# Kernel tuning notes

Hardware: AMD Instinct MI355X
Metric: run time of the kernel (lower is better)

## Reference

```python
import jax, jax.numpy as jnp
import numpy as np

NUM_HEADS = 16
ROPE_BASE = 50.0


def _apply_rope(x):
    # x: [b, s, h, d]; torchtune-style rotary embedding with base=ROPE_BASE
    b, s, h, d = x.shape
    inv_freq = 1.0 / (ROPE_BASE ** (jnp.arange(0, d, 2, dtype=jnp.float32) / d))  # [d/2]
    angles = jnp.arange(s, dtype=jnp.float32)[:, None] * inv_freq[None, :]         # [s, d/2]
    cos = jnp.cos(angles)[None, :, None, :]  # [1, s, 1, d/2]
    sin = jnp.sin(angles)[None, :, None, :]
    xr = x.reshape(b, s, h, d // 2, 2)
    x0, x1 = xr[..., 0], xr[..., 1]
    out = jnp.stack([x0 * cos - x1 * sin, x1 * cos + x0 * sin], axis=-1)
    return out.reshape(b, s, h, d).astype(x.dtype)


def setup_inputs() -> dict:
    key = jax.random.key(0)
    k1, k2, k3 = jax.random.split(key, 3)
    B, S, D = 2, 2048, 1024
    x = jax.random.normal(k1, (B, S, D), dtype=jnp.float32)
    w_qkv = jax.random.normal(k2, (3 * D, D), dtype=jnp.float32) * (D ** -0.5)
    w_out = jax.random.normal(k3, (D, D), dtype=jnp.float32) * (D ** -0.5)
    b_out = jnp.zeros((D,), dtype=jnp.float32)
    return {"x": x, "w_qkv": w_qkv, "w_out": w_out, "b_out": b_out}


def reference(x, w_qkv, w_out, b_out):
    B, S, D = x.shape
    H = NUM_HEADS
    dk = D // H

    qkv = x @ w_qkv.T                       # [b, s, 3D]
    q, k, v = jnp.split(qkv, 3, axis=-1)
    q = q.reshape(B, S, H, dk)
    k = k.reshape(B, S, H, dk)
    q = _apply_rope(q)
    k = _apply_rope(k)
    q = q.transpose(0, 2, 1, 3)             # [b, h, s, d]
    k = k.transpose(0, 2, 1, 3)
    v = v.reshape(B, S, H, dk).transpose(0, 2, 1, 3)

    scale = 1.0 / jnp.sqrt(jnp.asarray(dk, dtype=x.dtype))
    scores = jnp.einsum('bhsd,bhtd->bhst', q, k) * scale  # [b, h, s, s]
    # additive diagonal mask: -inf on the diagonal (blocks self-attention)
    eye = jnp.eye(S, dtype=bool)
    scores = jnp.where(eye[None, None], -jnp.inf, scores)
    attn = jax.nn.softmax(scores, axis=-1)
    out = jnp.einsum('bhst,bhtd->bhsd', attn, v)          # [b, h, s, d]
    out = out.transpose(0, 2, 1, 3).reshape(B, S, D)
    return out @ w_out.T + b_out
```

## Files before the change

kernel.cpp:

```cpp
#include <hip/hip_runtime.h>
#include <hip/hip_bf16.h>
#include <math.h>
#include <type_traits>

#define D_MODEL 1024
#define NHEADS  16
#define DK      64
#define SEQ     2048
#define BATCH   2
#define QTILE   128

typedef __attribute__((ext_vector_type(8)))  short  short8;
typedef __attribute__((ext_vector_type(8)))  unsigned short ushort8;
typedef __attribute__((ext_vector_type(4)))  float  floatx4;
typedef __attribute__((ext_vector_type(16))) float  floatx16;

__device__ __forceinline__ unsigned short f2bf(float f) {
    union { float f; unsigned int u; } v; v.f = f;
    unsigned int u = v.u;
    return (unsigned short)((u + 0x7FFFu + ((u >> 16) & 1u)) >> 16);
}
__device__ __forceinline__ float bf2f(unsigned short u) {
    union { unsigned int u; float f; } v; v.u = ((unsigned int)u) << 16;
    return v.f;
}
__device__ __forceinline__ unsigned int fau(float f) {
    union { float f; unsigned int u; } v; v.f = f; return v.u;
}

__device__ __forceinline__ void gload_lds16(const unsigned short* g, unsigned short* l) {
    __builtin_amdgcn_global_load_lds((__attribute__((address_space(1))) const void*)g,
                                     (__attribute__((address_space(3))) void*)l,
                                     16, 0, 0);
}

#define X8 ((BATCH * SEQ * D_MODEL) / 8)
#define W8 ((3 * D_MODEL * D_MODEL) / 8)
#define O8 ((D_MODEL * D_MODEL) / 8)
__global__ __launch_bounds__(256) void pack_all(const float* __restrict__ x,
                                                const float* __restrict__ wq,
                                                const float* __restrict__ wo,
                                                unsigned short* __restrict__ xb,
                                                unsigned short* __restrict__ wqb,
                                                unsigned short* __restrict__ wob) {
    const int t = blockIdx.x * blockDim.x + threadIdx.x;
    const float* src; unsigned short* dst; int idx;
    if (t < X8)           { src = x;  dst = xb;  idx = t; }
    else if (t < X8 + W8) { src = wq; dst = wqb; idx = t - X8; }
    else if (t < X8 + W8 + O8) { src = wo; dst = wob; idx = t - X8 - W8; }
    else return;
    const float4 a = ((const float4*)src)[2 * idx];
    const float4 b = ((const float4*)src)[2 * idx + 1];
    short8 o;
    o[0] = (short)f2bf(a.x); o[1] = (short)f2bf(a.y);
    o[2] = (short)f2bf(a.z); o[3] = (short)f2bf(a.w);
    o[4] = (short)f2bf(b.x); o[5] = (short)f2bf(b.y);
    o[6] = (short)f2bf(b.z); o[7] = (short)f2bf(b.w);
    ((short8*)dst)[idx] = o;
}

#define QKV_M 4096
#define QKV_N 3072
#define QKV_K 1024
#define QKV_NT (QKV_K / 64)

__global__ __launch_bounds__(512, 2) void gemm_qkv_8ph(const unsigned short* __restrict__ A,
                                                        const unsigned short* __restrict__ B,
                                                        unsigned short* __restrict__ C) {
    __shared__ __align__(16) unsigned short As[2][256][64];
    __shared__ __align__(16) unsigned short Bs[2][256][64];

    const int tid  = threadIdx.x;
    const int w    = tid >> 6;
    const int lane = tid & 63;
    const int quad = lane >> 4;
    const int lcol = lane & 15;
    const int wr   = w >> 2;
    const int wc   = w & 3;

    const int f  = blockIdx.x;
    const int wg = (f & 7) * 24 + (f >> 3);
    const int tn = (wg % (QKV_N / 256)) * 256;
    const int tm = (wg / (QKV_N / 256)) * 256;

    const int srow8 = lane >> 3;
    const int sj    = lane & 7;

    auto stageA = [&](int buf, int kt, int mh) {
#pragma unroll
        for (int c = 0; c < 2; ++c) {
            const int r0 = mh * 64 + c * 128 + w * 8;
            const int r  = r0 + srow8;
            gload_lds16(A + (size_t)(tm + r) * QKV_K + kt * 64 + ((sj ^ (r & 7)) * 8),
                        &As[buf][r0][0]);
        }
    };
    auto stageB = [&](int buf, int kt, int nh) {
#pragma unroll
        for (int c = 0; c < 2; ++c) {
            const int rho0 = c * 64 + w * 8;
            const int r0   = (rho0 >> 5) * 64 + nh * 32 + (rho0 & 31);
            const int r    = r0 + srow8;
            gload_lds16(B + (size_t)(tn + r) * QKV_K + kt * 64 + ((sj ^ (r & 7)) * 8),
                        &Bs[buf][r0][0]);
        }
    };

    floatx4 acc[8][4];
#pragma unroll
    for (int i = 0; i < 8; ++i)
#pragma unroll
        for (int j = 0; j < 4; ++j) acc[i][j] = (floatx4){0.f, 0.f, 0.f, 0.f};

    auto do_phase = [&](int buf, auto mhc, auto nhc, auto stager) {
        constexpr int mh = decltype(mhc)::value;
        constexpr int nh = decltype(nhc)::value;
        asm volatile("s_waitcnt vmcnt(4)" ::: "memory");
        __builtin_amdgcn_s_barrier();
        asm volatile("" ::: "memory");
        short8 a[4][2], bfr[2][2];
#pragma unroll
        for (int i = 0; i < 4; ++i)
#pragma unroll
            for (int kk = 0; kk < 2; ++kk) {
                const int r = wr * 128 + mh * 64 + i * 16 + lcol;
                a[i][kk] = *(const short8*)&As[buf][r][((kk * 4 + quad) ^ (r & 7)) * 8];
            }
#pragma unroll
        for (int j = 0; j < 2; ++j)
#pragma unroll
            for (int kk = 0; kk < 2; ++kk) {
                const int r = wc * 64 + nh * 32 + j * 16 + lcol;
                bfr[j][kk] = *(const short8*)&Bs[buf][r][((kk * 4 + quad) ^ (r & 7)) * 8];
            }
        stager();
        __builtin_amdgcn_s_setprio(1);
#pragma unroll
        for (int i = 0; i < 4; ++i)
#pragma unroll
            for (int j = 0; j < 2; ++j)
#pragma unroll
                for (int kk = 0; kk < 2; ++kk)
                    acc[mh * 4 + i][nh * 2 + j] = __builtin_amdgcn_mfma_f32_16x16x32_bf16(
                        a[i][kk], bfr[j][kk], acc[mh * 4 + i][nh * 2 + j], 0, 0, 0);
        __builtin_amdgcn_s_setprio(0);
    };

    using IC0 = std::integral_constant<int, 0>;
    using IC1 = std::integral_constant<int, 1>;

    stageA(0, 0, 0); stageB(0, 0, 0); stageB(0, 0, 1); stageA(0, 0, 1);

    for (int t = 0; t < QKV_NT; ++t) {
        const int buf = t & 1, nb = buf ^ 1;
        const int kn = (t + 1 == QKV_NT) ? 0 : t + 1;
        do_phase(buf, IC0{}, IC0{}, [&] { stageA(nb, kn, 0); });
        do_phase(buf, IC0{}, IC1{}, [&] { stageB(nb, kn, 0); });
        do_phase(buf, IC1{}, IC0{}, [&] { stageB(nb, kn, 1); });
        do_phase(buf, IC1{}, IC1{}, [&] { stageA(nb, kn, 1); });
    }

#pragma unroll
    for (int i = 0; i < 8; ++i) {
#pragma unroll
        for (int rr = 0; rr < 4; ++rr) {
            const int row = tm + wr * 128 + i * 16 + quad * 4 + rr;
#pragma unroll
            for (int jf = 0; jf < 4; ++jf) {
                const int col = tn + wc * 64 + jf * 16 + lcol;
                C[(size_t)row * QKV_N + col] = f2bf(acc[i][jf][rr]);
            }
        }
    }
}

#define OUT_M 4096
#define OUT_N 1024
#define OUT_K 1024
#define OUT_NT (OUT_K / 64)

__global__ __launch_bounds__(512, 2) void gemm_out_8ph(const unsigned short* __restrict__ A,
                                                       const unsigned short* __restrict__ B,
                                                       const float* __restrict__ bias,
                                                       float* __restrict__ C) {
    __shared__ __align__(16) unsigned short As[2][128][64];
    __shared__ __align__(16) unsigned short Bs[2][128][64];

    const int tid  = threadIdx.x;
    const int w    = tid >> 6;
    const int lane = tid & 63;
    const int quad = lane >> 4;
    const int lcol = lane & 15;
    const int wr   = w >> 2;
    const int wc   = w & 3;

    const int f  = blockIdx.x;
    const int wg = (f & 7) * 32 + (f >> 3);
    const int tn = (wg & 7) * 128;
    const int tm = (wg >> 3) * 128;

    const int srow8 = lane >> 3;
    const int sj    = lane & 7;

    auto stageA = [&](int buf, int kt, int mh) {
        const int r0 = (w & 3) * 8 + mh * 32 + (w >> 2) * 64;
        const int r  = r0 + srow8;
        gload_lds16(A + (size_t)(tm + r) * OUT_K + kt * 64 + ((sj ^ (r & 7)) * 8),
                    &As[buf][r0][0]);
    };
    auto stageB = [&](int buf, int kt, int nh) {
        const int r0 = (w >> 1) * 32 + nh * 16 + (w & 1) * 8;
        const int r  = r0 + srow8;
        gload_lds16(B + (size_t)(tn + r) * OUT_K + kt * 64 + ((sj ^ (r & 7)) * 8),
                    &Bs[buf][r0][0]);
    };

    floatx4 acc[4][2];
#pragma unroll
    for (int i = 0; i < 4; ++i)
#pragma unroll
        for (int j = 0; j < 2; ++j) acc[i][j] = (floatx4){0.f, 0.f, 0.f, 0.f};

    auto do_phase = [&](int buf, auto mhc, auto nhc, auto stager) {
        constexpr int mh = decltype(mhc)::value;
        constexpr int nh = decltype(nhc)::value;
        asm volatile("s_waitcnt vmcnt(2)" ::: "memory");
        __builtin_amdgcn_s_barrier();
        asm volatile("" ::: "memory");
        short8 a[2][2], bfr[2];
#pragma unroll
        for (int i = 0; i < 2; ++i)
#pragma unroll
            for (int kk = 0; kk < 2; ++kk) {
                const int r = wr * 64 + mh * 32 + i * 16 + lcol;
                a[i][kk] = *(const short8*)&As[buf][r][((kk * 4 + quad) ^ (r & 7)) * 8];
            }
#pragma unroll
        for (int kk = 0; kk < 2; ++kk) {
            const int r = wc * 32 + nh * 16 + lcol;
            bfr[kk] = *(const short8*)&Bs[buf][r][((kk * 4 + quad) ^ (r & 7)) * 8];
        }
        stager();
        __builtin_amdgcn_s_setprio(1);
#pragma unroll
        for (int i = 0; i < 2; ++i)
#pragma unroll
            for (int kk = 0; kk < 2; ++kk)
                acc[mh * 2 + i][nh] = __builtin_amdgcn_mfma_f32_16x16x32_bf16(
                    a[i][kk], bfr[kk], acc[mh * 2 + i][nh], 0, 0, 0);
        __builtin_amdgcn_s_setprio(0);
    };

    using IC0 = std::integral_constant<int, 0>;
    using IC1 = std::integral_constant<int, 1>;

    stageA(0, 0, 0); stageB(0, 0, 0); stageB(0, 0, 1); stageA(0, 0, 1);

    for (int t = 0; t < OUT_NT; ++t) {
        const int buf = t & 1, nb = buf ^ 1;
        const int kn = (t + 1 == OUT_NT) ? 0 : t + 1;
        do_phase(buf, IC0{}, IC0{}, [&] { stageA(nb, kn, 0); });
        do_phase(buf, IC0{}, IC1{}, [&] { stageB(nb, kn, 0); });
        do_phase(buf, IC1{}, IC0{}, [&] { stageB(nb, kn, 1); });
        do_phase(buf, IC1{}, IC1{}, [&] { stageA(nb, kn, 1); });
    }

#pragma unroll
    for (int i = 0; i < 4; ++i) {
#pragma unroll
        for (int rr = 0; rr < 4; ++rr) {
            const int row = tm + wr * 64 + i * 16 + quad * 4 + rr;
#pragma unroll
            for (int j = 0; j < 2; ++j) {
                const int col = tn + wc * 32 + j * 16 + lcol;
                C[(size_t)row * OUT_N + col] = acc[i][j][rr] + bias[col];
            }
        }
    }
}

__global__ __launch_bounds__(256) void rope_vtrans(const unsigned short* __restrict__ qkvb,
                                                   unsigned short* __restrict__ Qb,
                                                   unsigned short* __restrict__ Kb,
                                                   unsigned short* __restrict__ Vtg) {
    const int st = blockIdx.x, h = blockIdx.y, b = blockIdx.z;
    const int tid = threadIdx.x;
    const int s0 = st * 64;

    const int i  = tid & 31;
    const int r0 = tid >> 5;
    const float inv_freq = exp2f(-(2.0f * (float)i / (float)DK) * log2f(50.0f));
    const float QSCALE = 0.125f * 1.44269504f;
#pragma unroll
    for (int pass = 0; pass < 8; ++pass) {
        const int s = s0 + r0 + pass * 8;
        const size_t in_base = ((size_t)(b * SEQ + s)) * (3 * D_MODEL) + h * DK + 2 * i;
        const float q0 = bf2f(qkvb[in_base]),           q1 = bf2f(qkvb[in_base + 1]);
        const float k0 = bf2f(qkvb[in_base + D_MODEL]), k1 = bf2f(qkvb[in_base + D_MODEL + 1]);
        float sn, cs;
        __sincosf((float)s * inv_freq, &sn, &cs);
        const size_t ob = (((size_t)(b * NHEADS + h)) * SEQ + s) * DK + 2 * i;
        const unsigned int qw = (unsigned int)f2bf((q0 * cs - q1 * sn) * QSCALE)
                              | ((unsigned int)f2bf((q1 * cs + q0 * sn) * QSCALE) << 16);
        const unsigned int kw = (unsigned int)f2bf(k0 * cs - k1 * sn)
                              | ((unsigned int)f2bf(k1 * cs + k0 * sn) << 16);
        *(unsigned int*)&Qb[ob] = qw;
        *(unsigned int*)&Kb[ob] = kw;
    }

    __shared__ unsigned short Lt[64][65];
    const int r = tid >> 3;
    const int c = (tid & 7) * 8;
    const size_t in_row = ((size_t)(b * SEQ + s0 + r)) * (3 * D_MODEL) + 2 * D_MODEL + h * DK + c;
    const ushort8 v0 = *(const ushort8*)&qkvb[in_row];
    const ushort8 v1 = *(const ushort8*)&qkvb[in_row + (size_t)32 * (3 * D_MODEL)];
    const int u0 = r, u1 = r + 32;
    const int kc0 = (u0 & 48) | (8 * ((u0 >> 2) & 1) + (u0 & 3) + 4 * ((u0 >> 3) & 1));
    const int kc1 = (u1 & 48) | (8 * ((u1 >> 2) & 1) + (u1 & 3) + 4 * ((u1 >> 3) & 1));
#pragma unroll
    for (int j = 0; j < 8; ++j) Lt[c + j][kc0] = v0[j];
#pragma unroll
    for (int j = 0; j < 8; ++j) Lt[c + j][kc1] = v1[j];
    __syncthreads();
    const size_t bh = (size_t)(b * NHEADS + h);
    ushort8 o0, o1;
#pragma unroll
    for (int j = 0; j < 8; ++j) { o0[j] = Lt[r][c + j]; o1[j] = Lt[r + 32][c + j]; }
    unsigned short* orow = Vtg + (bh * DK + r) * SEQ + s0 + c;
    *(ushort8*)orow = o0;
    *(ushort8*)(orow + (size_t)32 * SEQ) = o1;
}

#define LDW 72

__global__ __launch_bounds__(512, 4) void flash_attn(const unsigned short* __restrict__ Qb,
                                                     const unsigned short* __restrict__ Kb,
                                                     const unsigned short* __restrict__ Vtg,
                                                     unsigned short* __restrict__ attnb) {
    const int tid  = threadIdx.x;
    const int wave = tid >> 6;
    const int lane = tid & 63;
    const int l31  = lane & 31;
    const int lh   = lane >> 5;
    const int mh2  = wave & 3;
    const int kh   = wave >> 2;
    const int kb   = kh * 32;

    const int f  = blockIdx.x + gridDim.x * (blockIdx.y + gridDim.y * blockIdx.z);
    const int w  = (f & 7) * 64 + (f >> 3);
    const int qt = w & 15;
    const int h  = (w >> 4) & 15;
    const int b  = w >> 8;

    __shared__ __align__(16) unsigned char smem[36864];
    unsigned short (*Ks0)[LDW] = (unsigned short (*)[LDW])(smem);
    unsigned short (*Vt0)[LDW] = (unsigned short (*)[LDW])(smem +  9216);
    unsigned short (*Ks1)[LDW] = (unsigned short (*)[LDW])(smem + 18432);
    unsigned short (*Vt1)[LDW] = (unsigned short (*)[LDW])(smem + 27648);
    float (*Ored)[68] = (float (*)[68])smem;
    float* lred0 = (float*)(smem + 34816);
    float* lred1 = lred0 + 128;

    const size_t bh = (size_t)(b * NHEADS + h);
    const unsigned short* Qg = Qb + (bh * SEQ + (size_t)qt * QTILE) * DK;
    const unsigned short* Kg = Kb + bh * SEQ * DK;
    const unsigned short* Vg = Vtg + bh * (size_t)DK * SEQ;

    short8 qf[4];
#pragma unroll
    for (int t = 0; t < 4; ++t)
        qf[t] = *(const short8*)&Qg[(size_t)(mh2 * 32 + l31) * DK + t * 16 + lh * 8];

    const int strow = tid >> 3;
    const int stcol = (tid & 7) * 8;
    const unsigned short* kg = &Kg[(size_t)strow * DK + stcol];
    const unsigned short* vg = &Vg[(size_t)strow * SEQ + stcol];

    short8 kr = *(const short8*)&kg[0];
    short8 vr = *(const short8*)&vg[0];

    floatx16 oacc[2];
    oacc[0] = (floatx16)(0.f);
    oacc[1] = (floatx16)(0.f);
    float lp = 0.f;

    const int diagkt = qt * QTILE + mh2 * 32 - kb;

    auto compute = [&](unsigned short (*Ks)[LDW], unsigned short (*Vt)[LDW], int kt) {
        floatx16 sc = (floatx16)(0.f);
        __builtin_amdgcn_s_setprio(1);
#pragma unroll
        for (int t = 0; t < 4; ++t) {
            const short8 kf = *(short8*)&Ks[kb + l31][t * 16 + lh * 8];
            sc = __builtin_amdgcn_mfma_f32_32x32x16_bf16(kf, qf[t], sc, 0, 0, 0);
        }
        __builtin_amdgcn_s_setprio(0);

        if (kt == diagkt) {
#pragma unroll
            for (int r = 0; r < 16; ++r) {
                const int key_loc = (r & 3) + 8 * (r >> 2) + 4 * lh;
                if (key_loc == l31) sc[r] = -1e30f;
            }
        }

        short8 pf0, pf1;
        {
            union { unsigned int u[4]; short8 s8; } a, c;
#pragma unroll
            for (int d = 0; d < 4; ++d) {
                const float e0 = __builtin_amdgcn_exp2f(sc[2 * d]);
                const float e1 = __builtin_amdgcn_exp2f(sc[2 * d + 1]);
                a.u[d] = __builtin_amdgcn_perm(fau(e1), fau(e0), 0x07060302u);
                const float f0 = __builtin_amdgcn_exp2f(sc[8 + 2 * d]);
                const float f1 = __builtin_amdgcn_exp2f(sc[8 + 2 * d + 1]);
                c.u[d] = __builtin_amdgcn_perm(fau(f1), fau(f0), 0x07060302u);
                lp += (e0 + e1) + (f0 + f1);
            }
            pf0 = a.s8;
            pf1 = c.s8;
        }

        __builtin_amdgcn_s_setprio(1);
#pragma unroll
        for (int nd = 0; nd < 2; ++nd) {
            const short8 vfa = *(short8*)&Vt[nd * 32 + l31][kb + lh * 8];
            const short8 vfb = *(short8*)&Vt[nd * 32 + l31][kb + 16 + lh * 8];
            oacc[nd] = __builtin_amdgcn_mfma_f32_32x32x16_bf16(pf0, vfa, oacc[nd], 0, 0, 0);
            oacc[nd] = __builtin_amdgcn_mfma_f32_32x32x16_bf16(pf1, vfb, oacc[nd], 0, 0, 0);
        }
        __builtin_amdgcn_s_setprio(0);
    };

    for (int kt = 0; kt < SEQ; kt += 128) {
        *(short8*)&Ks0[strow][stcol] = kr;
        *(short8*)&Vt0[strow][stcol] = vr;
        __syncthreads();
        kr = *(const short8*)&kg[(size_t)(kt + 64) * DK];
        vr = *(const short8*)&vg[kt + 64];
        compute(Ks0, Vt0, kt);

        *(short8*)&Ks1[strow][stcol] = kr;
        *(short8*)&Vt1[strow][stcol] = vr;
        __syncthreads();
        const int ktn = (kt + 128 < SEQ) ? kt + 128 : 0;
        kr = *(const short8*)&kg[(size_t)ktn * DK];
        vr = *(const short8*)&vg[ktn];
        compute(Ks1, Vt1, kt + 64);
    }

    const float lptot = lp + __shfl_xor(lp, 32, 64);

    __syncthreads();
    if (lh == 0) {
        if (kh == 0) lred0[mh2 * 32 + l31] = lptot;
        else         lred1[mh2 * 32 + l31] = lptot;
    }
    if (kh == 1) {
#pragma unroll
        for (int r = 0; r < 16; ++r) {
            const int m = mh2 * 32 + (r & 3) + 8 * (r >> 2) + 4 * lh;
            Ored[m][l31]      = oacc[0][r];
            Ored[m][32 + l31] = oacc[1][r];
        }
    }
    __syncthreads();
    if (kh == 0) {
        unsigned short* obase = attnb + ((size_t)b * SEQ + (size_t)qt * QTILE) * D_MODEL + h * DK;
#pragma unroll
        for (int r = 0; r < 16; ++r) {
            const int m = mh2 * 32 + (r & 3) + 8 * (r >> 2) + 4 * lh;
            const float inv = 1.001953125f / (lred0[m] + lred1[m]);
            const float v0 = (oacc[0][r] + Ored[m][l31]) * inv;
            const float v1 = (oacc[1][r] + Ored[m][32 + l31]) * inv;
            obase[(size_t)m * D_MODEL + l31]      = f2bf(v0);
            obase[(size_t)m * D_MODEL + 32 + l31] = f2bf(v1);
        }
    }
}

extern "C" void kernel_launch(void* const* d_in, const int* in_sizes, int n_in,
                              void* d_out, int out_size, void* d_ws, size_t ws_size,
                              hipStream_t stream) {
    const float* x     = (const float*)d_in[0];
    const float* w_qkv = (const float*)d_in[1];
    const float* w_out = (const float*)d_in[2];
    const float* b_out = (const float*)d_in[3];
    float* out = (float*)d_out;

    const int M = BATCH * SEQ;
    const size_t X_ELEMS    = (size_t)M * D_MODEL;
    const size_t WQKV_ELEMS = (size_t)3 * D_MODEL * D_MODEL;
    const size_t WOUT_ELEMS = (size_t)D_MODEL * D_MODEL;
    const size_t QKV_ELEMS  = (size_t)M * 3 * D_MODEL;
    const size_t HEAD_ELEMS = (size_t)BATCH * NHEADS * SEQ * DK;

    unsigned short* xb    = (unsigned short*)d_ws;
    unsigned short* wqkvb = xb + X_ELEMS;
    unsigned short* woutb = wqkvb + WQKV_ELEMS;
    unsigned short* qkvb  = woutb + WOUT_ELEMS;
    unsigned short* Qb    = qkvb + QKV_ELEMS;
    unsigned short* Kb    = Qb + HEAD_ELEMS;
    unsigned short* Vtg   = Kb + HEAD_ELEMS;
    unsigned short* attnb = Vtg + HEAD_ELEMS;

    pack_all<<<(X8 + W8 + O8 + 255) / 256, 256, 0, stream>>>(x, w_qkv, w_out, xb, wqkvb, woutb);

    gemm_qkv_8ph<<<(QKV_M / 256) * (QKV_N / 256), 512, 0, stream>>>(xb, wqkvb, qkvb);

    {
        dim3 grid(SEQ / 64, NHEADS, BATCH);
        rope_vtrans<<<grid, 256, 0, stream>>>(qkvb, Qb, Kb, Vtg);
    }
    {
        dim3 grid(SEQ / QTILE, NHEADS, BATCH);
        flash_attn<<<grid, 512, 0, stream>>>(Qb, Kb, Vtg, attnb);
    }
    gemm_out_8ph<<<(OUT_M / 128) * (OUT_N / 128), 512, 0, stream>>>(attnb, woutb, b_out, out);
}
```

Baseline: 185.0 us.

## Split GEMM phases by k-half and software-pipeline QK^T with softmax-PV in attention

```diff
diff --git a/kernel.cpp b/kernel.cpp
--- a/kernel.cpp
+++ b/kernel.cpp
@@ -14,6 +14,8 @@
 typedef __attribute__((ext_vector_type(8)))  unsigned short ushort8;
 typedef __attribute__((ext_vector_type(4)))  float  floatx4;
 typedef __attribute__((ext_vector_type(16))) float  floatx16;
+
+template <int N> using IC = std::integral_constant<int, N>;
 
 __device__ __forceinline__ unsigned short f2bf(float f) {
     union { float f; unsigned int u; } v; v.f = f;
@@ -112,52 +114,45 @@
 #pragma unroll
         for (int j = 0; j < 4; ++j) acc[i][j] = (floatx4){0.f, 0.f, 0.f, 0.f};
 
-    auto do_phase = [&](int buf, auto mhc, auto nhc, auto stager) {
+    auto do_phase = [&](int buf, auto vmc, auto kkc, auto mhc, auto stager) {
+        constexpr int VM = decltype(vmc)::value;
+        constexpr int kk = decltype(kkc)::value;
         constexpr int mh = decltype(mhc)::value;
-        constexpr int nh = decltype(nhc)::value;
-        asm volatile("s_waitcnt vmcnt(4)" ::: "memory");
+        if constexpr (VM == 2) asm volatile("s_waitcnt vmcnt(2)" ::: "memory");
+        else                   asm volatile("s_waitcnt vmcnt(4)" ::: "memory");
         __builtin_amdgcn_s_barrier();
         asm volatile("" ::: "memory");
-        short8 a[4][2], bfr[2][2];
-#pragma unroll
-        for (int i = 0; i < 4; ++i)
-#pragma unroll
-            for (int kk = 0; kk < 2; ++kk) {
-                const int r = wr * 128 + mh * 64 + i * 16 + lcol;
-                a[i][kk] = *(const short8*)&As[buf][r][((kk * 4 + quad) ^ (r & 7)) * 8];
-            }
-#pragma unroll
-        for (int j = 0; j < 2; ++j)
-#pragma unroll
-            for (int kk = 0; kk < 2; ++kk) {
-                const int r = wc * 64 + nh * 32 + j * 16 + lcol;
-                bfr[j][kk] = *(const short8*)&Bs[buf][r][((kk * 4 + quad) ^ (r & 7)) * 8];
-            }
+        short8 a[4], b[4];
+#pragma unroll
+        for (int i = 0; i < 4; ++i) {
+            const int r = wr * 128 + mh * 64 + i * 16 + lcol;
+            a[i] = *(const short8*)&As[buf][r][((kk * 4 + quad) ^ (r & 7)) * 8];
+        }
+#pragma unroll
+        for (int j = 0; j < 4; ++j) {
+            const int r = wc * 64 + j * 16 + lcol;
+            b[j] = *(const short8*)&Bs[buf][r][((kk * 4 + quad) ^ (r & 7)) * 8];
+        }
         stager();
         __builtin_amdgcn_s_setprio(1);
 #pragma unroll
         for (int i = 0; i < 4; ++i)
 #pragma unroll
-            for (int j = 0; j < 2; ++j)
-#pragma unroll
-                for (int kk = 0; kk < 2; ++kk)
-                    acc[mh * 4 + i][nh * 2 + j] = __builtin_amdgcn_mfma_f32_16x16x32_bf16(
-                        a[i][kk], bfr[j][kk], acc[mh * 4 + i][nh * 2 + j], 0, 0, 0);
+            for (int j = 0; j < 4; ++j)
+                acc[mh * 4 + i][j] = __builtin_amdgcn_mfma_f32_16x16x32_bf16(
+                    a[i], b[j], acc[mh * 4 + i][j], 0, 0, 0);
         __builtin_amdgcn_s_setprio(0);
     };
 
-    using IC0 = std::integral_constant<int, 0>;
-    using IC1 = std::integral_constant<int, 1>;
-
-    stageA(0, 0, 0); stageB(0, 0, 0); stageB(0, 0, 1); stageA(0, 0, 1);
+    stageB(0, 0, 0); stageB(0, 0, 1); stageA(0, 0, 0); stageA(0, 0, 1);
 
     for (int t = 0; t < QKV_NT; ++t) {
         const int buf = t & 1, nb = buf ^ 1;
         const int kn = (t + 1 == QKV_NT) ? 0 : t + 1;
-        do_phase(buf, IC0{}, IC0{}, [&] { stageA(nb, kn, 0); });
-        do_phase(buf, IC0{}, IC1{}, [&] { stageB(nb, kn, 0); });
-        do_phase(buf, IC1{}, IC0{}, [&] { stageB(nb, kn, 1); });
-        do_phase(buf, IC1{}, IC1{}, [&] { stageA(nb, kn, 1); });
+        do_phase(buf, IC<2>{}, IC<0>{}, IC<0>{}, [&] { stageB(nb, kn, 0); });
+        do_phase(buf, IC<2>{}, IC<0>{}, IC<1>{}, [&] { stageB(nb, kn, 1); });
+        do_phase(buf, IC<4>{}, IC<1>{}, IC<0>{}, [&] { stageA(nb, kn, 0); });
+        do_phase(buf, IC<4>{}, IC<1>{}, IC<1>{}, [&] { stageA(nb, kn, 1); });
     }
 
 #pragma unroll
@@ -221,48 +216,45 @@
 #pragma unroll
         for (int j = 0; j < 2; ++j) acc[i][j] = (floatx4){0.f, 0.f, 0.f, 0.f};
 
-    auto do_phase = [&](int buf, auto mhc, auto nhc, auto stager) {
+    auto do_phase = [&](int buf, auto vmc, auto kkc, auto mhc, auto stager) {
+        constexpr int VM = decltype(vmc)::value;
+        constexpr int kk = decltype(kkc)::value;
         constexpr int mh = decltype(mhc)::value;
-        constexpr int nh = decltype(nhc)::value;
-        asm volatile("s_waitcnt vmcnt(2)" ::: "memory");
+        if constexpr (VM == 1) asm volatile("s_waitcnt vmcnt(1)" ::: "memory");
+        else                   asm volatile("s_waitcnt vmcnt(2)" ::: "memory");
         __builtin_amdgcn_s_barrier();
         asm volatile("" ::: "memory");
-        short8 a[2][2], bfr[2];
-#pragma unroll
-        for (int i = 0; i < 2; ++i)
-#pragma unroll
-            for (int kk = 0; kk < 2; ++kk) {
-                const int r = wr * 64 + mh * 32 + i * 16 + lcol;
-                a[i][kk] = *(const short8*)&As[buf][r][((kk * 4 + quad) ^ (r & 7)) * 8];
-            }
-#pragma unroll
-        for (int kk = 0; kk < 2; ++kk) {
-            const int r = wc * 32 + nh * 16 + lcol;
-            bfr[kk] = *(const short8*)&Bs[buf][r][((kk * 4 + quad) ^ (r & 7)) * 8];
+        short8 a[2], b[2];
+#pragma unroll
+        for (int i = 0; i < 2; ++i) {
+            const int r = wr * 64 + mh * 32 + i * 16 + lcol;
+            a[i] = *(const short8*)&As[buf][r][((kk * 4 + quad) ^ (r & 7)) * 8];
+        }
+#pragma unroll
+        for (int j = 0; j < 2; ++j) {
+            const int r = wc * 32 + j * 16 + lcol;
+            b[j] = *(const short8*)&Bs[buf][r][((kk * 4 + quad) ^ (r & 7)) * 8];
         }
         stager();
         __builtin_amdgcn_s_setprio(1);
 #pragma unroll
         for (int i = 0; i < 2; ++i)
 #pragma unroll
-            for (int kk = 0; kk < 2; ++kk)
-                acc[mh * 2 + i][nh] = __builtin_amdgcn_mfma_f32_16x16x32_bf16(
-                    a[i][kk], bfr[kk], acc[mh * 2 + i][nh], 0, 0, 0);
+            for (int j = 0; j < 2; ++j)
+                acc[mh * 2 + i][j] = __builtin_amdgcn_mfma_f32_16x16x32_bf16(
+                    a[i], b[j], acc[mh * 2 + i][j], 0, 0, 0);
         __builtin_amdgcn_s_setprio(0);
     };
 
-    using IC0 = std::integral_constant<int, 0>;
-    using IC1 = std::integral_constant<int, 1>;
-
-    stageA(0, 0, 0); stageB(0, 0, 0); stageB(0, 0, 1); stageA(0, 0, 1);
+    stageB(0, 0, 0); stageB(0, 0, 1); stageA(0, 0, 0); stageA(0, 0, 1);
 
     for (int t = 0; t < OUT_NT; ++t) {
         const int buf = t & 1, nb = buf ^ 1;
         const int kn = (t + 1 == OUT_NT) ? 0 : t + 1;
-        do_phase(buf, IC0{}, IC0{}, [&] { stageA(nb, kn, 0); });
-        do_phase(buf, IC0{}, IC1{}, [&] { stageB(nb, kn, 0); });
-        do_phase(buf, IC1{}, IC0{}, [&] { stageB(nb, kn, 1); });
-        do_phase(buf, IC1{}, IC1{}, [&] { stageA(nb, kn, 1); });
+        do_phase(buf, IC<1>{}, IC<0>{}, IC<0>{}, [&] { stageB(nb, kn, 0); });
+        do_phase(buf, IC<1>{}, IC<0>{}, IC<1>{}, [&] { stageB(nb, kn, 1); });
+        do_phase(buf, IC<2>{}, IC<1>{}, IC<0>{}, [&] { stageA(nb, kn, 0); });
+        do_phase(buf, IC<2>{}, IC<1>{}, IC<1>{}, [&] { stageA(nb, kn, 1); });
     }
 
 #pragma unroll
@@ -352,11 +344,9 @@
     const int h  = (w >> 4) & 15;
     const int b  = w >> 8;
 
-    __shared__ __align__(16) unsigned char smem[36864];
-    unsigned short (*Ks0)[LDW] = (unsigned short (*)[LDW])(smem);
-    unsigned short (*Vt0)[LDW] = (unsigned short (*)[LDW])(smem +  9216);
-    unsigned short (*Ks1)[LDW] = (unsigned short (*)[LDW])(smem + 18432);
-    unsigned short (*Vt1)[LDW] = (unsigned short (*)[LDW])(smem + 27648);
+    __shared__ __align__(16) unsigned char smem[55296];
+    auto KsAt = [&](int s) { return (unsigned short (*)[LDW])(smem + s * 18432); };
+    auto VtAt = [&](int s) { return (unsigned short (*)[LDW])(smem + s * 18432 + 9216); };
     float (*Ored)[68] = (float (*)[68])smem;
     float* lred0 = (float*)(smem + 34816);
     float* lred1 = lred0 + 128;
@@ -386,41 +376,30 @@
 
     const int diagkt = qt * QTILE + mh2 * 32 - kb;
 
-    auto compute = [&](unsigned short (*Ks)[LDW], unsigned short (*Vt)[LDW], int kt) {
-        floatx16 sc = (floatx16)(0.f);
-        __builtin_amdgcn_s_setprio(1);
-#pragma unroll
-        for (int t = 0; t < 4; ++t) {
-            const short8 kf = *(short8*)&Ks[kb + l31][t * 16 + lh * 8];
-            sc = __builtin_amdgcn_mfma_f32_32x32x16_bf16(kf, qf[t], sc, 0, 0, 0);
-        }
-        __builtin_amdgcn_s_setprio(0);
-
+    auto finishP = [&](floatx16 s, int kt, unsigned short (*Vt)[LDW]) {
         if (kt == diagkt) {
 #pragma unroll
             for (int r = 0; r < 16; ++r) {
                 const int key_loc = (r & 3) + 8 * (r >> 2) + 4 * lh;
-                if (key_loc == l31) sc[r] = -1e30f;
+                if (key_loc == l31) s[r] = -1e30f;
             }
         }
-
         short8 pf0, pf1;
         {
             union { unsigned int u[4]; short8 s8; } a, c;
 #pragma unroll
             for (int d = 0; d < 4; ++d) {
-                const float e0 = __builtin_amdgcn_exp2f(sc[2 * d]);
-                const float e1 = __builtin_amdgcn_exp2f(sc[2 * d + 1]);
+                const float e0 = __builtin_amdgcn_exp2f(s[2 * d]);
+                const float e1 = __builtin_amdgcn_exp2f(s[2 * d + 1]);
                 a.u[d] = __builtin_amdgcn_perm(fau(e1), fau(e0), 0x07060302u);
-                const float f0 = __builtin_amdgcn_exp2f(sc[8 + 2 * d]);
-                const float f1 = __builtin_amdgcn_exp2f(sc[8 + 2 * d + 1]);
+                const float f0 = __builtin_amdgcn_exp2f(s[8 + 2 * d]);
+                const float f1 = __builtin_amdgcn_exp2f(s[8 + 2 * d + 1]);
                 c.u[d] = __builtin_amdgcn_perm(fau(f1), fau(f0), 0x07060302u);
                 lp += (e0 + e1) + (f0 + f1);
             }
             pf0 = a.s8;
             pf1 = c.s8;
         }
-
         __builtin_amdgcn_s_setprio(1);
 #pragma unroll
         for (int nd = 0; nd < 2; ++nd) {
@@ -432,22 +411,32 @@
         __builtin_amdgcn_s_setprio(0);
     };
 
-    for (int kt = 0; kt < SEQ; kt += 128) {
-        *(short8*)&Ks0[strow][stcol] = kr;
-        *(short8*)&Vt0[strow][stcol] = vr;
+    floatx16 scp;
+    int bs = 0, bsp = 0;
+    for (int j = 0; j < 32; ++j) {
+        unsigned short (*Ks)[LDW] = KsAt(bs);
+        *(short8*)&Ks[strow][stcol]        = kr;
+        *(short8*)&VtAt(bs)[strow][stcol]  = vr;
         __syncthreads();
-        kr = *(const short8*)&kg[(size_t)(kt + 64) * DK];
-        vr = *(const short8*)&vg[kt + 64];
-        compute(Ks0, Vt0, kt);
-
-        *(short8*)&Ks1[strow][stcol] = kr;
-        *(short8*)&Vt1[strow][stcol] = vr;
-        __syncthreads();
-        const int ktn = (kt + 128 < SEQ) ? kt + 128 : 0;
+        const int ktn = (j + 1 < 32) ? (j + 1) * 64 : 0;
         kr = *(const short8*)&kg[(size_t)ktn * DK];
         vr = *(const short8*)&vg[ktn];
-        compute(Ks1, Vt1, kt + 64);
-    }
+
+        floatx16 sc = (floatx16)(0.f);
+        __builtin_amdgcn_s_setprio(1);
+#pragma unroll
+        for (int t = 0; t < 4; ++t) {
+            const short8 kf = *(short8*)&Ks[kb + l31][t * 16 + lh * 8];
+            sc = __builtin_amdgcn_mfma_f32_32x32x16_bf16(kf, qf[t], sc, 0, 0, 0);
+        }
+        __builtin_amdgcn_s_setprio(0);
+
+        if (j > 0) finishP(scp, (j - 1) * 64, VtAt(bsp));
+        scp = sc;
+        bsp = bs;
+        bs  = (bs == 2) ? 0 : bs + 1;
+    }
+    finishP(scp, 31 * 64, VtAt(bsp));
 
     const float lptot = lp + __shfl_xor(lp, 32, 64);
 
```

New measurement: 184.5 us. About the same (-0.3%).
